# Performance work log

Hardware: AMD Instinct MI355X
Metric: run time of the kernel (lower is better)

## Reference

```python
import jax, jax.numpy as jnp
import numpy as np

N_NODES = 100000

def gcn_conv(x, edge_index, W, b, n_nodes):
    # GCNConv: out = D^{-1/2} (A + I) D^{-1/2} X W + b  (self-loops added)
    src, dst = edge_index[0], edge_index[1]
    loops = jnp.arange(n_nodes, dtype=edge_index.dtype)
    src = jnp.concatenate([src, loops])
    dst = jnp.concatenate([dst, loops])
    deg = jax.ops.segment_sum(jnp.ones_like(dst, dtype=x.dtype), dst, num_segments=n_nodes)
    dinv = jnp.where(deg > 0, jax.lax.rsqrt(deg), 0.0)
    norm = dinv[src] * dinv[dst]  # [E+N]
    h = x @ W  # transform first (small d), then gather/scatter
    msgs = h[src] * norm[:, None]
    out = jax.ops.segment_sum(msgs, dst, num_segments=n_nodes)
    return out + b


def setup_inputs() -> dict:
    key = jax.random.key(0)
    k1, k2, k3, k4, k5, k6 = jax.random.split(key, 6)
    x = jax.random.normal(k1, (N_NODES, 3), dtype=jnp.float32)
    edge_index = jax.random.randint(k2, (2, 2400000), 0, N_NODES, dtype=jnp.int64)
    # Glorot-style init for GCNConv linear weights; zero bias matches PyG default
    W1 = jax.random.normal(k3, (3, 16), dtype=jnp.float32) * (1.0 / np.sqrt(3))
    b1 = jnp.zeros((16,), dtype=jnp.float32)
    W2 = jax.random.normal(k4, (16, 32), dtype=jnp.float32) * (1.0 / np.sqrt(16))
    b2 = jnp.zeros((32,), dtype=jnp.float32)
    return {"x": x, "edge_index": edge_index, "W1": W1, "b1": b1, "W2": W2, "b2": b2}


def reference(x, edge_index, W1, b1, W2, b2):
    n = x.shape[0]
    h = gcn_conv(x, edge_index, W1, b1, n)
    h = jax.nn.relu(h)
    h = gcn_conv(h, edge_index, W2, b2, n)
    # batch is all zeros in the original forward -> single-graph mean pool
    return jnp.mean(h, axis=0, keepdims=True)  # [1, 32]
```

## Files before the change

kernel.cpp:

```cpp
#include <hip/hip_runtime.h>

typedef unsigned int uint;
typedef unsigned long long ull;


#define MAXB  256
#define CAP   16384u
#define BINB  512
#define CHUNK 4096
#define SPL   8
#define PADN  131072
#define AFS   2048.0f
#define AFB   16384
#define AFM   0x1FFFFFu

__device__ __forceinline__ uint slice_lo(uint c, uint s) {
    return (s == 0u) ? 0u : ((c * s / SPL) & ~7u);
}
__device__ __forceinline__ uint slice_hi(uint c, uint s) {
    return (s == SPL - 1u) ? c : ((c * (s + 1u) / SPL) & ~7u);
}

__global__ void __launch_bounds__(BINB)
bin_kernel(const int* __restrict__ key, const int* __restrict__ other,
           uint* __restrict__ cursor, uint* __restrict__ buf, int E) {
    __shared__ uint cnt[MAXB], scanb[MAXB], baseb[MAXB];
    __shared__ uint stage[CHUNK];
    const int tid = threadIdx.x;
    const int e0 = blockIdx.x * CHUNK;
    const int nE = min(CHUNK, E - e0);
    const int my0 = tid * 8;
    const int myc = max(0, min(8, nE - my0));
    if (tid < MAXB) cnt[tid] = 0u;

    uint k8[8], o8[8], r8[8];
    if (myc == 8) {
        int4 ka = ((const int4*)(key + e0))[tid * 2];
        int4 kb = ((const int4*)(key + e0))[tid * 2 + 1];
        int4 oa = ((const int4*)(other + e0))[tid * 2];
        int4 ob = ((const int4*)(other + e0))[tid * 2 + 1];
        k8[0] = ka.x; k8[1] = ka.y; k8[2] = ka.z; k8[3] = ka.w;
        k8[4] = kb.x; k8[5] = kb.y; k8[6] = kb.z; k8[7] = kb.w;
        o8[0] = oa.x; o8[1] = oa.y; o8[2] = oa.z; o8[3] = oa.w;
        o8[4] = ob.x; o8[5] = ob.y; o8[6] = ob.z; o8[7] = ob.w;
    } else {
        for (int r = 0; r < myc; ++r) {
            k8[r] = (uint)key[e0 + my0 + r];
            o8[r] = (uint)other[e0 + my0 + r];
        }
    }
    __syncthreads();
    for (int r = 0; r < myc; ++r) r8[r] = atomicAdd(&cnt[k8[r] >> 9], 1u);
    __syncthreads();
    if (tid < MAXB) scanb[tid] = cnt[tid];
    __syncthreads();
    for (int d = 1; d < MAXB; d <<= 1) {
        uint t = (tid < MAXB && tid >= d) ? scanb[tid - d] : 0u;
        __syncthreads();
        if (tid < MAXB) scanb[tid] += t;
        __syncthreads();
    }
    if (tid < MAXB) baseb[tid] = (uint)tid * CAP + (cnt[tid] ? atomicAdd(&cursor[tid * 16], cnt[tid]) : 0u);
    __syncthreads();
    for (int r = 0; r < myc; ++r) {
        uint b = k8[r] >> 9;
        stage[(scanb[b] - cnt[b]) + r8[r]] = ((k8[r] & 511u) << 17) | o8[r];
    }
    __syncthreads();
    const int wave = tid >> 6, lane = tid & 63;
    for (int b = wave; b < MAXB; b += BINB / 64) {
        uint s0 = scanb[b] - cnt[b], c = cnt[b], gb = baseb[b];
        uint lim = (uint)(b + 1) * CAP;
        for (uint i = lane; i < c; i += 64u) {
            uint gp = gb + i;
            if (gp < lim) buf[gp] = stage[s0 + i];
        }
    }
}

__global__ void __launch_bounds__(256)
deg_kernel(const uint* __restrict__ buf, const uint* __restrict__ curD,
           uint* __restrict__ degg, int n) {
    __shared__ uint dg[512];
    const int tid = threadIdx.x;
    const int b = blockIdx.x >> 3;
    const uint s = blockIdx.x & 7;
    const uint base = (uint)b * CAP;
    const uint c = min(curD[b * 16], CAP);
    const uint lo = slice_lo(c, s), hi = slice_hi(c, s);
    dg[tid] = 0u; dg[tid + 256] = 0u;
    __syncthreads();
    for (uint i0 = lo + (uint)tid * 8u; i0 < hi; i0 += 2048u) {
        uint cnt8 = min(8u, hi - i0);
        uint en[8];
        if (cnt8 == 8u) {
            uint4 a = ((const uint4*)(buf + base + i0))[0];
            uint4 bb = ((const uint4*)(buf + base + i0))[1];
            en[0] = a.x; en[1] = a.y; en[2] = a.z; en[3] = a.w;
            en[4] = bb.x; en[5] = bb.y; en[6] = bb.z; en[7] = bb.w;
        } else {
            for (uint r = 0; r < cnt8; ++r) en[r] = buf[base + i0 + r];
        }
        for (uint r = 0; r < cnt8; ++r) atomicAdd(&dg[en[r] >> 17], 1u);
    }
    __syncthreads();
    for (int t = tid; t < 512; t += 256) {
        int node = (b << 9) + t;
        if (node < n && dg[t]) atomicAdd(&degg[node], dg[t]);
    }
}

__global__ void node1_kernel(const float* __restrict__ x, const uint* __restrict__ degg,
                             float* __restrict__ dinv, float4* __restrict__ xd4, int n) {
    int i = blockIdx.x * blockDim.x + threadIdx.x;
    if (i >= n) return;
    float di = rsqrtf((float)(degg[i] + 1u));
    dinv[i] = di;
    xd4[i] = make_float4(x[3 * i] * di, x[3 * i + 1] * di, x[3 * i + 2] * di, di);
}

__global__ void __launch_bounds__(256)
agg_kernel(const uint* __restrict__ buf, const uint* __restrict__ curD,
           const float4* __restrict__ xd4, ull* __restrict__ accp, int n) {
    __shared__ ull acc[512];
    const int tid = threadIdx.x;
    const int b = blockIdx.x >> 3;
    const uint s = blockIdx.x & 7;
    const uint base = (uint)b * CAP;
    const uint c = min(curD[b * 16], CAP);
    const uint lo = slice_lo(c, s), hi = slice_hi(c, s);
    acc[tid] = 0ull; acc[tid + 256] = 0ull;
    __syncthreads();
    for (uint i0 = lo + (uint)tid * 8u; i0 < hi + 8u * 2048u; i0 += 2048u) {
        if (i0 >= hi) continue;
        uint cnt8 = min(8u, hi - i0);
        uint en[8];
        if (cnt8 == 8u) {
            uint4 a = ((const uint4*)(buf + base + i0))[0];
            uint4 bb = ((const uint4*)(buf + base + i0))[1];
            en[0] = a.x; en[1] = a.y; en[2] = a.z; en[3] = a.w;
            en[4] = bb.x; en[5] = bb.y; en[6] = bb.z; en[7] = bb.w;
        } else {
            for (uint r = 0; r < cnt8; ++r) en[r] = buf[base + i0 + r];
            for (uint r = cnt8; r < 8u; ++r) en[r] = en[0];
        }
        float4 gv[8];
#pragma unroll
        for (int r = 0; r < 8; ++r) gv[r] = xd4[en[r] & 0x1FFFFu];
#pragma unroll
        for (uint r = 0; r < 8u; ++r) {
            if (r < cnt8) {
                uint dl = en[r] >> 17;
                ull f0 = (ull)(uint)((int)rintf(gv[r].x * AFS) + AFB);
                ull f1 = (ull)(uint)((int)rintf(gv[r].y * AFS) + AFB);
                ull f2 = (ull)(uint)((int)rintf(gv[r].z * AFS) + AFB);
                atomicAdd(&acc[dl], f0 | (f1 << 21) | (f2 << 42));
            }
        }
    }
    __syncthreads();
    for (int t = tid; t < 512; t += 256) {
        ull v = acc[t];
        int node = (b << 9) + t;
        if (v && node < n) atomicAdd(&accp[node], v);
    }
}

__global__ void __launch_bounds__(256)
q_kernel(const ull* __restrict__ accp, const uint* __restrict__ degg,
         const float4* __restrict__ xd4, const float* __restrict__ W1,
         const float* __restrict__ b1, uint4* __restrict__ qb,
         float* __restrict__ T, int n) {
    __shared__ float tacc[16];
    const int tid = threadIdx.x;
    if (tid < 16) tacc[tid] = 0.0f;
    __syncthreads();
    int i = blockIdx.x * blockDim.x + tid;
    float sq[16];
    if (i < n) {
        float4 sv = xd4[i];
        float di = sv.w;
        ull v = accp[i];
        int ub = (int)(degg[i] * (uint)AFB);
        const float isc = 1.0f / AFS;
        float a = (float)((int)(uint)(v & AFM) - ub) * isc + sv.x;
        float b = (float)((int)(uint)((v >> 21) & AFM) - ub) * isc + sv.y;
        float c = (float)((int)(uint)((v >> 42) & AFM) - ub) * isc + sv.z;
        float q[16];
#pragma unroll
        for (int k = 0; k < 16; ++k) {
            float h = di * (a * W1[k] + b * W1[16 + k] + c * W1[32 + k]) + b1[k];
            h = fmaxf(h, 0.0f);
            q[k] = di * h;
            sq[k] = di * q[k];
        }
        uint pk[8];
#pragma unroll
        for (int k = 0; k < 8; ++k) {
            uint l = __float_as_uint(q[2 * k]);
            l = (l + 0x7FFFu + ((l >> 16) & 1u)) >> 16;
            uint h2 = __float_as_uint(q[2 * k + 1]);
            h2 = ((h2 + 0x7FFFu + ((h2 >> 16) & 1u)) & 0xFFFF0000u);
            pk[k] = l | h2;
        }
        qb[2 * (size_t)i]     = make_uint4(pk[0], pk[1], pk[2], pk[3]);
        qb[2 * (size_t)i + 1] = make_uint4(pk[4], pk[5], pk[6], pk[7]);
    } else {
#pragma unroll
        for (int k = 0; k < 16; ++k) sq[k] = 0.0f;
    }
#pragma unroll
    for (int k = 0; k < 16; ++k) {
        float v = sq[k];
        for (int off = 32; off > 0; off >>= 1) v += __shfl_down(v, off, 64);
        if ((tid & 63) == 0) atomicAdd(&tacc[k], v);
    }
    __syncthreads();
    if (tid < 16) atomicAdd(&T[tid], tacc[tid]);
}

__global__ void __launch_bounds__(256)
T_kernel(const uint* __restrict__ buf, const uint* __restrict__ curD,
         const float* __restrict__ dinv, const uint4* __restrict__ qb,
         float* __restrict__ T, int n) {
    __shared__ float dt[512];
    __shared__ float tacc[16];
    const int tid = threadIdx.x;
    const int b = blockIdx.x >> 3;
    const uint s = blockIdx.x & 7;
    const uint base = (uint)b * CAP;
    const uint c = min(curD[b * 16], CAP);
    const uint lo = slice_lo(c, s), hi = slice_hi(c, s);
    for (int t = tid; t < 512; t += 256) {
        int node = (b << 9) + t;
        dt[t] = (node < n) ? dinv[node] : 0.0f;
    }
    if (tid < 16) tacc[tid] = 0.0f;
    __syncthreads();
    float rac[16];
#pragma unroll
    for (int k = 0; k < 16; ++k) rac[k] = 0.0f;
    for (uint i0 = lo + (uint)tid * 8u; i0 < hi + 8u * 2048u; i0 += 2048u) {
        if (i0 >= hi) continue;
        uint cnt8 = min(8u, hi - i0);
        uint en[8];
        if (cnt8 == 8u) {
            uint4 a = ((const uint4*)(buf + base + i0))[0];
            uint4 bb = ((const uint4*)(buf + base + i0))[1];
            en[0] = a.x; en[1] = a.y; en[2] = a.z; en[3] = a.w;
            en[4] = bb.x; en[5] = bb.y; en[6] = bb.z; en[7] = bb.w;
        } else {
            for (uint r = 0; r < cnt8; ++r) en[r] = buf[base + i0 + r];
            for (uint r = cnt8; r < 8u; ++r) en[r] = en[0];
        }
        uint4 qa[8], qc[8];
#pragma unroll
        for (int r = 0; r < 8; ++r) {
            uint sv = en[r] & 0x1FFFFu;
            qa[r] = qb[2 * (size_t)sv];
            qc[r] = qb[2 * (size_t)sv + 1];
        }
#pragma unroll
        for (uint r = 0; r < 8u; ++r) {
            if (r < cnt8) {
                float di = dt[en[r] >> 17];
                uint w[8] = {qa[r].x, qa[r].y, qa[r].z, qa[r].w,
                             qc[r].x, qc[r].y, qc[r].z, qc[r].w};
#pragma unroll
                for (int k = 0; k < 8; ++k) {
                    rac[2 * k]     += di * __uint_as_float(w[k] << 16);
                    rac[2 * k + 1] += di * __uint_as_float(w[k] & 0xFFFF0000u);
                }
            }
        }
    }
#pragma unroll
    for (int k = 0; k < 16; ++k) {
        float v = rac[k];
        for (int off = 32; off > 0; off >>= 1) v += __shfl_down(v, off, 64);
        if ((tid & 63) == 0) atomicAdd(&tacc[k], v);
    }
    __syncthreads();
    if (tid < 16) atomicAdd(&T[tid], tacc[tid]);
}

__global__ void out_kernel(const float* __restrict__ T, const float* __restrict__ W2,
                           const float* __restrict__ b2, float* __restrict__ out, float invN) {
    int j = threadIdx.x;
    float s = 0.0f;
#pragma unroll
    for (int k = 0; k < 16; ++k) s += T[k] * W2[k * 32 + j];
    out[j] = b2[j] + invN * s;
}

extern "C" void kernel_launch(void* const* d_in, const int* in_sizes, int n_in,
                              void* d_out, int out_size, void* d_ws, size_t ws_size,
                              hipStream_t stream) {
    const float* x   = (const float*)d_in[0];
    const int*   ei  = (const int*)d_in[1];
    const float* W1  = (const float*)d_in[2];
    const float* b1  = (const float*)d_in[3];
    const float* W2  = (const float*)d_in[4];
    const float* b2  = (const float*)d_in[5];
    float* out = (float*)d_out;

    const int n = in_sizes[0] / 3;
    const int E = in_sizes[1] / 2;
    const int* src = ei;
    const int* dst = ei + E;

    char* p = (char*)d_ws;
    float* T    = (float*)p;    p += 64;
    uint*  curD = (uint*)p;     p += MAXB * 16 * 4;
    uint*  degg = (uint*)p;     p += (size_t)n * 4;
    ull*   accp = (ull*)p;      p += (size_t)n * 8;
    size_t zbytes = (size_t)(p - (char*)d_ws);
    uint*   bufD  = (uint*)p;   p += (size_t)MAXB * CAP * 4;
    float*  dinv  = (float*)p;  p += (size_t)n * 4;
    p = (char*)(((size_t)p + 31) & ~(size_t)31);
    float4* xd4   = (float4*)p; p += (size_t)PADN * 16;
    uint4*  qb    = (uint4*)p;  p += (size_t)PADN * 32;

    const int nb = (n + 511) >> 9;

    hipMemsetAsync(d_ws, 0, zbytes, stream);
    bin_kernel<<<(E + CHUNK - 1) / CHUNK, BINB, 0, stream>>>(dst, src, curD, bufD, E);
    deg_kernel<<<nb * SPL, 256, 0, stream>>>(bufD, curD, degg, n);
    node1_kernel<<<(n + 255) / 256, 256, 0, stream>>>(x, degg, dinv, xd4, n);
    agg_kernel<<<nb * SPL, 256, 0, stream>>>(bufD, curD, xd4, accp, n);
    q_kernel<<<(n + 255) / 256, 256, 0, stream>>>(accp, degg, xd4, W1, b1, qb, T, n);
    T_kernel<<<nb * SPL, 256, 0, stream>>>(bufD, curD, dinv, qb, T, n);
    out_kernel<<<1, 32, 0, stream>>>(T, W2, b2, out, 1.0f / (float)n);
}
```

Before: 167.5 us.

## Store layer-1 features as FP8, fuse output into T_kernel, shrink memset

Packs the 16-wide per-node hidden features as scaled FP8 (16 bytes per node) instead of BF16 (32 bytes), which halves the random-gather traffic in T_kernel. It also folds the final 32-wide output projection into T_kernel with a last-block atomic counter, and moves the zeroing of degg/accp into bin_kernel so the memset only covers a small header. The cost is lower precision in the gathered features and reliance on bin_kernel's grid covering all n nodes for zeroing.

```diff
diff --git a/kernel.cpp b/kernel.cpp
--- a/kernel.cpp
+++ b/kernel.cpp
@@ -13,6 +13,8 @@
 #define AFS   2048.0f
 #define AFB   16384
 #define AFM   0x1FFFFFu
+#define QS    16.0f
+#define QSI   0.0625f
 
 __device__ __forceinline__ uint slice_lo(uint c, uint s) {
     return (s == 0u) ? 0u : ((c * s / SPL) & ~7u);
@@ -23,10 +25,15 @@
 
 __global__ void __launch_bounds__(BINB)
 bin_kernel(const int* __restrict__ key, const int* __restrict__ other,
-           uint* __restrict__ cursor, uint* __restrict__ buf, int E) {
+           uint* __restrict__ cursor, uint* __restrict__ buf,
+           uint* __restrict__ degg, ull* __restrict__ accp, int n, int E) {
     __shared__ uint cnt[MAXB], scanb[MAXB], baseb[MAXB];
     __shared__ uint stage[CHUNK];
     const int tid = threadIdx.x;
+    {
+        int gz = blockIdx.x * BINB + tid;
+        if (gz < n) { degg[gz] = 0u; accp[gz] = 0ull; }
+    }
     const int e0 = blockIdx.x * CHUNK;
     const int nE = min(CHUNK, E - e0);
     const int my0 = tid * 8;
@@ -194,17 +201,13 @@
             q[k] = di * h;
             sq[k] = di * q[k];
         }
-        uint pk[8];
-#pragma unroll
-        for (int k = 0; k < 8; ++k) {
-            uint l = __float_as_uint(q[2 * k]);
-            l = (l + 0x7FFFu + ((l >> 16) & 1u)) >> 16;
-            uint h2 = __float_as_uint(q[2 * k + 1]);
-            h2 = ((h2 + 0x7FFFu + ((h2 >> 16) & 1u)) & 0xFFFF0000u);
-            pk[k] = l | h2;
-        }
-        qb[2 * (size_t)i]     = make_uint4(pk[0], pk[1], pk[2], pk[3]);
-        qb[2 * (size_t)i + 1] = make_uint4(pk[4], pk[5], pk[6], pk[7]);
+        int w[4] = {0, 0, 0, 0};
+#pragma unroll
+        for (int m = 0; m < 4; ++m) {
+            w[m] = __builtin_amdgcn_cvt_pk_fp8_f32(q[4 * m] * QS, q[4 * m + 1] * QS, w[m], false);
+            w[m] = __builtin_amdgcn_cvt_pk_fp8_f32(q[4 * m + 2] * QS, q[4 * m + 3] * QS, w[m], true);
+        }
+        qb[i] = make_uint4((uint)w[0], (uint)w[1], (uint)w[2], (uint)w[3]);
     } else {
 #pragma unroll
         for (int k = 0; k < 16; ++k) sq[k] = 0.0f;
@@ -222,9 +225,12 @@
 __global__ void __launch_bounds__(256)
 T_kernel(const uint* __restrict__ buf, const uint* __restrict__ curD,
          const float* __restrict__ dinv, const uint4* __restrict__ qb,
-         float* __restrict__ T, int n) {
+         float* __restrict__ T, uint* __restrict__ tcount,
+         const float* __restrict__ W2, const float* __restrict__ b2,
+         float* __restrict__ out, int n, int nblk, float invN) {
     __shared__ float dt[512];
     __shared__ float tacc[16];
+    __shared__ uint isLast;
     const int tid = threadIdx.x;
     const int b = blockIdx.x >> 3;
     const uint s = blockIdx.x & 7;
@@ -253,23 +259,22 @@
             for (uint r = 0; r < cnt8; ++r) en[r] = buf[base + i0 + r];
             for (uint r = cnt8; r < 8u; ++r) en[r] = en[0];
         }
-        uint4 qa[8], qc[8];
-#pragma unroll
-        for (int r = 0; r < 8; ++r) {
-            uint sv = en[r] & 0x1FFFFu;
-            qa[r] = qb[2 * (size_t)sv];
-            qc[r] = qb[2 * (size_t)sv + 1];
-        }
+        uint4 qv[8];
+#pragma unroll
+        for (int r = 0; r < 8; ++r) qv[r] = qb[en[r] & 0x1FFFFu];
 #pragma unroll
         for (uint r = 0; r < 8u; ++r) {
             if (r < cnt8) {
                 float di = dt[en[r] >> 17];
-                uint w[8] = {qa[r].x, qa[r].y, qa[r].z, qa[r].w,
-                             qc[r].x, qc[r].y, qc[r].z, qc[r].w};
-#pragma unroll
-                for (int k = 0; k < 8; ++k) {
-                    rac[2 * k]     += di * __uint_as_float(w[k] << 16);
-                    rac[2 * k + 1] += di * __uint_as_float(w[k] & 0xFFFF0000u);
+                uint w[4] = {qv[r].x, qv[r].y, qv[r].z, qv[r].w};
+#pragma unroll
+                for (int m = 0; m < 4; ++m) {
+                    auto p0 = __builtin_amdgcn_cvt_pk_f32_fp8((int)w[m], false);
+                    auto p1 = __builtin_amdgcn_cvt_pk_f32_fp8((int)w[m], true);
+                    rac[4 * m]     += di * p0[0];
+                    rac[4 * m + 1] += di * p0[1];
+                    rac[4 * m + 2] += di * p1[0];
+                    rac[4 * m + 3] += di * p1[1];
                 }
             }
         }
@@ -281,16 +286,23 @@
         if ((tid & 63) == 0) atomicAdd(&tacc[k], v);
     }
     __syncthreads();
-    if (tid < 16) atomicAdd(&T[tid], tacc[tid]);
-}
-
-__global__ void out_kernel(const float* __restrict__ T, const float* __restrict__ W2,
-                           const float* __restrict__ b2, float* __restrict__ out, float invN) {
-    int j = threadIdx.x;
-    float s = 0.0f;
-#pragma unroll
-    for (int k = 0; k < 16; ++k) s += T[k] * W2[k * 32 + j];
-    out[j] = b2[j] + invN * s;
+    if (tid < 16) atomicAdd(&T[tid], tacc[tid] * QSI);
+    __threadfence();
+    if (tid == 0) {
+        uint prev = atomicAdd(tcount, 1u);
+        isLast = (prev == (uint)(nblk - 1)) ? 1u : 0u;
+    }
+    __syncthreads();
+    if (isLast) {
+        if (tid < 16) tacc[tid] = atomicAdd(&T[tid], 0.0f);
+        __syncthreads();
+        if (tid < 32) {
+            float sum = 0.0f;
+#pragma unroll
+            for (int k = 0; k < 16; ++k) sum += tacc[k] * W2[k * 32 + tid];
+            out[tid] = b2[tid] + invN * sum;
+        }
+    }
 }
 
 extern "C" void kernel_launch(void* const* d_in, const int* in_sizes, int n_in,
@@ -310,25 +322,26 @@
     const int* dst = ei + E;
 
     char* p = (char*)d_ws;
-    float* T    = (float*)p;    p += 64;
-    uint*  curD = (uint*)p;     p += MAXB * 16 * 4;
-    uint*  degg = (uint*)p;     p += (size_t)n * 4;
-    ull*   accp = (ull*)p;      p += (size_t)n * 8;
+    float* T      = (float*)p;  p += 64;
+    uint*  tcount = (uint*)p;   p += 64;
+    uint*  curD   = (uint*)p;   p += MAXB * 16 * 4;
     size_t zbytes = (size_t)(p - (char*)d_ws);
+    uint*   degg  = (uint*)p;   p += (size_t)n * 4;
+    ull*    accp  = (ull*)p;    p += (size_t)n * 8;
     uint*   bufD  = (uint*)p;   p += (size_t)MAXB * CAP * 4;
     float*  dinv  = (float*)p;  p += (size_t)n * 4;
     p = (char*)(((size_t)p + 31) & ~(size_t)31);
     float4* xd4   = (float4*)p; p += (size_t)PADN * 16;
-    uint4*  qb    = (uint4*)p;  p += (size_t)PADN * 32;
+    uint4*  qb    = (uint4*)p;  p += (size_t)PADN * 16;
 
     const int nb = (n + 511) >> 9;
+    const int nblkT = nb * SPL;
 
     hipMemsetAsync(d_ws, 0, zbytes, stream);
-    bin_kernel<<<(E + CHUNK - 1) / CHUNK, BINB, 0, stream>>>(dst, src, curD, bufD, E);
+    bin_kernel<<<(E + CHUNK - 1) / CHUNK, BINB, 0, stream>>>(dst, src, curD, bufD, degg, accp, n, E);
     deg_kernel<<<nb * SPL, 256, 0, stream>>>(bufD, curD, degg, n);
     node1_kernel<<<(n + 255) / 256, 256, 0, stream>>>(x, degg, dinv, xd4, n);
     agg_kernel<<<nb * SPL, 256, 0, stream>>>(bufD, curD, xd4, accp, n);
     q_kernel<<<(n + 255) / 256, 256, 0, stream>>>(accp, degg, xd4, W1, b1, qb, T, n);
-    T_kernel<<<nb * SPL, 256, 0, stream>>>(bufD, curD, dinv, qb, T, n);
-    out_kernel<<<1, 32, 0, stream>>>(T, W2, b2, out, 1.0f / (float)n);
-}
+    T_kernel<<<nblkT, 256, 0, stream>>>(bufD, curD, dinv, qb, T, tcount, W2, b2, out, n, nblkT, 1.0f / (float)n);
+}
```

After: 243.9 us. 45.6% more time.
